# Optimization experiments

Hardware: AMD Instinct MI355X
Metric: run time of the kernel (lower is better)

The kernel has to match this reference:

```python
import jax, jax.numpy as jnp
import numpy as np

B, S, D, H = 2, 2048, 1024, 16
DEPTH = D // H


def setup_inputs() -> dict:
    key = jax.random.key(0)
    ks = jax.random.split(key, 6)
    q = jax.random.normal(ks[0], (B, S, D), dtype=jnp.float32)
    k = jax.random.normal(ks[1], (B, S, D), dtype=jnp.float32)
    v = jax.random.normal(ks[2], (B, S, D), dtype=jnp.float32)
    # causal mask, broadcastable to [B, H, S, S]
    mask = jnp.tril(jnp.ones((S, S), dtype=bool))[None, None, :, :]
    wq = jax.random.normal(ks[3], (D, D), dtype=jnp.float32)
    wk = jax.random.normal(ks[4], (D, D), dtype=jnp.float32)
    wv = jax.random.normal(ks[5], (D, D), dtype=jnp.float32)
    return {"q": q, "k": k, "v": v, "mask": mask, "wq": wq, "wk": wk, "wv": wv}


def _split_heads(x):
    # [B, S, D] -> [B, H, S, depth]
    return x.reshape(x.shape[0], -1, H, DEPTH).transpose(0, 2, 1, 3)


def reference(q, k, v, mask, wq, wk, wv):
    q = _split_heads(q @ wq)
    k = _split_heads(k @ wk)
    v = _split_heads(v @ wv)
    scale = jnp.sqrt(jnp.float32(DEPTH))
    # [B, H, S, S]
    scores = jnp.einsum("bhqd,bhkd->bhqk", q, k) / scale
    scores = jnp.where(mask, scores, jnp.float32(-8.0))
    scores = scores - jnp.max(scores, axis=-1, keepdims=True)
    attn = jax.nn.softmax(scores, axis=-1)
    out = jnp.einsum("bhqk,bhkd->bhqd", attn, v)
    # [B, H, S, depth] -> [B, S, D]
    return out.transpose(0, 2, 1, 3).reshape(out.shape[0], -1, D)
```

## Files before the change

### kernel.cpp

```cpp
#include <hip/hip_runtime.h>
#include <hip/hip_bf16.h>

#define B_  2
#define S_  2048
#define D_  1024
#define H_  16
#define DH_ 64

typedef __attribute__((ext_vector_type(8)))  short  short8;
typedef __attribute__((ext_vector_type(4)))  short  short4b;
typedef __attribute__((ext_vector_type(16))) float  f32x16;

#define MFMA32(A,B,C) __builtin_amdgcn_mfma_f32_32x32x16_bf16(A,B,C,0,0,0)

static __device__ __forceinline__ short bf16b(float x) {
    __hip_bfloat16 h = __float2bfloat16(x);
    return *(short*)&h;
}
static __device__ __forceinline__ float bf16tof(short s) {
    union { unsigned u; float f; } cv;
    cv.u = ((unsigned)(unsigned short)s) << 16;
    return cv.f;
}
static __device__ __forceinline__ void gl2lds(const short* g, short* l) {
    __builtin_amdgcn_global_load_lds(
        (const __attribute__((address_space(1))) unsigned int*)g,
        (__attribute__((address_space(3))) unsigned int*)l, 16, 0, 0);
}

__global__ __launch_bounds__(256)
void conv_x(const float* __restrict__ q, const float* __restrict__ k,
            const float* __restrict__ v, char* __restrict__ ws) {
    const int z = blockIdx.y;
    const float* src = z == 0 ? q : z == 1 ? k : v;
    short* hi = (short*)(ws + (size_t)z * 16777216);
    short* lo = hi + 4194304;
    const int i = (blockIdx.x * 256 + threadIdx.x) * 4;
    float4 xv = *(const float4*)&src[i];
    const float* xf = (const float*)&xv;
    short4b h4, l4;
#pragma unroll
    for (int e = 0; e < 4; ++e) {
        short hb = bf16b(xf[e]);
        h4[e] = hb;
        l4[e] = bf16b(xf[e] - bf16tof(hb));
    }
    *(short4b*)&hi[i] = h4;
    *(short4b*)&lo[i] = l4;
}

__global__ __launch_bounds__(256)
void conv_wT(const float* __restrict__ wq, const float* __restrict__ wk,
             const float* __restrict__ wv, char* __restrict__ ws) {
    __shared__ short HiT[64][80];
    __shared__ short LoT[64][80];
    const int z = blockIdx.z;
    const float* w = z == 0 ? wq : z == 1 ? wk : wv;
    short* oh = (short*)(ws + 50331648 + (size_t)z * 4194304);
    short* ol = oh + 1048576;
    const int t  = threadIdx.x;
    const int k0 = blockIdx.x * 64, n0 = blockIdx.y * 64;

    const int kr = t >> 2, c4 = (t & 3) * 16;
    const float* srow = w + (size_t)(k0 + kr) * 1024 + n0 + c4;
#pragma unroll
    for (int u = 0; u < 16; u += 4) {
        float4 f = *(const float4*)&srow[u];
        const float* ff = (const float*)&f;
#pragma unroll
        for (int e = 0; e < 4; ++e) {
            int nl = c4 + u + e;
            short hb = bf16b(ff[e]);
            HiT[nl][kr] = hb;
            LoT[nl][kr] = bf16b(ff[e] - bf16tof(hb));
        }
    }
    __syncthreads();
    const int nl = t >> 2, kc = (t & 3) * 16;
    size_t off = (size_t)(n0 + nl) * 1024 + k0 + kc;
    *(short8*)&oh[off]     = *(const short8*)&HiT[nl][kc];
    *(short8*)&oh[off + 8] = *(const short8*)&HiT[nl][kc + 8];
    *(short8*)&ol[off]     = *(const short8*)&LoT[nl][kc];
    *(short8*)&ol[off + 8] = *(const short8*)&LoT[nl][kc + 8];
}

#define AHI_ 0
#define ALO_ 4096
#define BHI_ 8192
#define BLO_ 12288

__global__ __launch_bounds__(256, 2)
void proj_mfma(const short* __restrict__ xh0, const short* __restrict__ xl0,
               const short* __restrict__ xh1, const short* __restrict__ xl1,
               const short* __restrict__ xh2, const short* __restrict__ xl2,
               const short* __restrict__ wh0, const short* __restrict__ wl0,
               const short* __restrict__ wh1, const short* __restrict__ wl1,
               const short* __restrict__ wh2, const short* __restrict__ wl2,
               short* __restrict__ qh, short* __restrict__ ql,
               short* __restrict__ kh, short* __restrict__ kl,
               short* __restrict__ vt) {
    __shared__ short lds[16384];
    const int z  = blockIdx.z;
    const int m0 = blockIdx.y * 128;
    const int n0 = blockIdx.x * 128;
    const int t = threadIdx.x, lane = t & 63, w = t >> 6;
    const int l31 = lane & 31, hh = lane >> 5;

    const short* xh = z == 0 ? xh0 : z == 1 ? xh1 : xh2;
    const short* xl = z == 0 ? xl0 : z == 1 ? xl1 : xl2;
    const short* wh = z == 0 ? wh0 : z == 1 ? wh1 : wh2;
    const short* wl = z == 0 ? wl0 : z == 1 ? wl1 : wl2;

    const short* gsrc[8];
    short*       ldst[8];
#pragma unroll
    for (int j = 0; j < 8; ++j) {
        int sub = ((j & 1) << 2) | w;
        int cc  = (sub << 6) | lane;
        int row = cc >> 2, p = cc & 3;
        int kc  = p ^ ((row & 3) ^ ((row >> 2) & 3));
        bool isA  = j < 4;
        bool isHi = (j & 2) == 0;
        const short* base = isA ? (isHi ? xh : xl) : (isHi ? wh : wl);
        int r0g = isA ? m0 : n0;
        gsrc[j] = base + (size_t)(r0g + row) * 1024 + kc * 8;
        ldst[j] = &lds[(j >> 1) * 4096 + sub * 512];
    }

    const int rm0 = ((w & 1) << 6) + l31, rm1 = rm0 + 32;
    const int rn0 = ((w >> 1) << 6) + l31, rn1 = rn0 + 32;
    const int swm = (rm0 & 3) ^ ((rm0 >> 2) & 3);
    const int swn = (rn0 & 3) ^ ((rn0 >> 2) & 3);

    f32x16 accs[2][2] = {};

    for (int kt = 0; kt < 32; ++kt) {
        __syncthreads();
#pragma unroll
        for (int j = 0; j < 8; ++j)
            gl2lds(gsrc[j] + kt * 32, ldst[j]);
        __syncthreads();
#pragma unroll
        for (int ks = 0; ks < 2; ++ks) {
            const int kc = (ks << 1) | hh;
            const int om = (kc ^ swm) << 3;
            const int on = (kc ^ swn) << 3;
            short8 ah0 = *(const short8*)&lds[AHI_ + rm0 * 32 + om];
            short8 ah1 = *(const short8*)&lds[AHI_ + rm1 * 32 + om];
            short8 al0 = *(const short8*)&lds[ALO_ + rm0 * 32 + om];
            short8 al1 = *(const short8*)&lds[ALO_ + rm1 * 32 + om];
            short8 bh0 = *(const short8*)&lds[BHI_ + rn0 * 32 + on];
            short8 bh1 = *(const short8*)&lds[BHI_ + rn1 * 32 + on];
            short8 bl0 = *(const short8*)&lds[BLO_ + rn0 * 32 + on];
            short8 bl1 = *(const short8*)&lds[BLO_ + rn1 * 32 + on];
            accs[0][0] = MFMA32(ah0, bh0, accs[0][0]);
            accs[0][0] = MFMA32(ah0, bl0, accs[0][0]);
            accs[0][0] = MFMA32(al0, bh0, accs[0][0]);
            accs[0][1] = MFMA32(ah0, bh1, accs[0][1]);
            accs[0][1] = MFMA32(ah0, bl1, accs[0][1]);
            accs[0][1] = MFMA32(al0, bh1, accs[0][1]);
            accs[1][0] = MFMA32(ah1, bh0, accs[1][0]);
            accs[1][0] = MFMA32(ah1, bl0, accs[1][0]);
            accs[1][0] = MFMA32(al1, bh0, accs[1][0]);
            accs[1][1] = MFMA32(ah1, bh1, accs[1][1]);
            accs[1][1] = MFMA32(ah1, bl1, accs[1][1]);
            accs[1][1] = MFMA32(al1, bh1, accs[1][1]);
        }
    }

    const int qm = w & 1, qn = w >> 1;
    const int bb = m0 >> 11;
    const int sbase = (m0 & 2047) + qm * 64;
    if (z < 2) {
        short* oh = z == 0 ? qh : kh;
        short* ol = z == 0 ? ql : kl;
#pragma unroll
        for (int mt = 0; mt < 2; ++mt)
#pragma unroll
        for (int nt = 0; nt < 2; ++nt) {
            int n_g = n0 + qn * 64 + nt * 32 + l31;
            int h = n_g >> 6, d = n_g & 63;
#pragma unroll
            for (int r = 0; r < 16; ++r) {
                int s = sbase + mt * 32 + (r & 3) + 8 * (r >> 2) + 4 * hh;
                size_t off = (((size_t)(bb * 16 + h) * 2048 + s) << 6) + d;
                float a = accs[mt][nt][r];
                short hb = bf16b(a);
                oh[off] = hb;
                ol[off] = bf16b(a - bf16tof(hb));
            }
        }
    } else {
#pragma unroll
        for (int mt = 0; mt < 2; ++mt)
#pragma unroll
        for (int nt = 0; nt < 2; ++nt) {
            int n_g = n0 + qn * 64 + nt * 32 + l31;
            int h = n_g >> 6, d = n_g & 63;
            size_t vbase = ((size_t)(bb * 16 + h) * 64 + d) * 2048;
#pragma unroll
            for (int r2 = 0; r2 < 4; ++r2) {
                int s0 = sbase + mt * 32 + 8 * r2 + 4 * hh;
                short4b pk;
#pragma unroll
                for (int a2 = 0; a2 < 4; ++a2)
                    pk[a2] = bf16b(accs[mt][nt][r2 * 4 + a2]);
                *(short4b*)&vt[vbase + s0] = pk;
            }
        }
    }
}

__global__ void vtile_sums(const short* __restrict__ Vt, float* __restrict__ TS) {
    int c = blockIdx.x, bh = blockIdx.y, d = threadIdx.x;
    const short* row = Vt + ((size_t)bh * DH_ + d) * S_ + c * 64;
    float s = 0.f;
    for (int j = 0; j < 64; ++j) s += bf16tof(row[j]);
    TS[((size_t)bh * 32 + c) * 64 + d] = s;
}

__global__ void suffix_scan(const float* __restrict__ TS, float* __restrict__ SV) {
    int bh = blockIdx.x, d = threadIdx.x;
    float run = 0.f;
    for (int c = 32; c >= 0; --c) {
        SV[((size_t)bh * 33 + c) * 64 + d] = run;
        if (c > 0) run += TS[((size_t)bh * 32 + (c - 1)) * 64 + d];
    }
}

__global__ __launch_bounds__(256, 2)
void attn_mfma(const short* __restrict__ Qhi, const short* __restrict__ Qlo,
               const short* __restrict__ Khi, const short* __restrict__ Klo,
               const short* __restrict__ Vt,  const float* __restrict__ SV,
               float* __restrict__ out) {
    __shared__ __align__(16) short KhiS[64 * 72];
    __shared__ __align__(16) short KloS[64 * 72];
    __shared__ __align__(16) short VtS [64 * 72];
    __shared__ __align__(16) short PS  [4][32 * 72];

    const int t     = threadIdx.x;
    const int lane  = t & 63;
    const int w     = t >> 6;
    const int l31   = lane & 31;
    const int hh    = lane >> 5;
    const int bh    = blockIdx.x;
    const int yy    = blockIdx.y;
    const int qt    = (yy < 8) ? yy : 23 - yy;
    const int q0    = qt * 128;
    const int myq   = q0 + w * 32 + l31;
    const int ktend = 2 * qt + 2;

    const size_t basebh = (size_t)bh * S_ * DH_;

    short8 qh[4], ql[4];
    {
        const short* qr = Qhi + basebh + (size_t)myq * DH_;
        const short* lr = Qlo + basebh + (size_t)myq * DH_;
#pragma unroll
        for (int kf = 0; kf < 4; ++kf) {
            int dofs = kf * 16 + hh * 8;
            qh[kf] = *(const short8*)(qr + dofs);
            ql[kf] = *(const short8*)(lr + dofs);
        }
    }

    float m_run = -INFINITY, l_run = 0.f;
    f32x16 oT0 = {}, oT1 = {};

    const int srow = t >> 2;
    const int sc16 = (t & 3) * 16;

    for (int kt = 0; kt < ktend; ++kt) {
        __syncthreads();
        {
            const short* gH = Khi + basebh + (size_t)(kt * 64 + srow) * 64 + sc16;
            const short* gL = Klo + basebh + (size_t)(kt * 64 + srow) * 64 + sc16;
            const short* gV = Vt + (size_t)bh * DH_ * S_ + (size_t)srow * S_ + kt * 64 + sc16;
            short8 a0 = *(const short8*)gH, a1 = *(const short8*)(gH + 8);
            short8 b0 = *(const short8*)gL, b1 = *(const short8*)(gL + 8);
            short8 c0 = *(const short8*)gV, c1 = *(const short8*)(gV + 8);
            *(short8*)&KhiS[srow * 72 + sc16]     = a0;
            *(short8*)&KhiS[srow * 72 + sc16 + 8] = a1;
            *(short8*)&KloS[srow * 72 + sc16]     = b0;
            *(short8*)&KloS[srow * 72 + sc16 + 8] = b1;
            *(short8*)&VtS [srow * 72 + sc16]     = c0;
            *(short8*)&VtS [srow * 72 + sc16 + 8] = c1;
        }
        __syncthreads();

        f32x16 acc0 = {}, acc1 = {};
#pragma unroll
        for (int kf = 0; kf < 4; ++kf) {
            int dofs = kf * 16 + hh * 8;
            short8 k0h = *(const short8*)&KhiS[(l31)      * 72 + dofs];
            short8 k0l = *(const short8*)&KloS[(l31)      * 72 + dofs];
            short8 k1h = *(const short8*)&KhiS[(l31 + 32) * 72 + dofs];
            short8 k1l = *(const short8*)&KloS[(l31 + 32) * 72 + dofs];
            acc0 = MFMA32(k0h, qh[kf], acc0);
            acc0 = MFMA32(k0h, ql[kf], acc0);
            acc0 = MFMA32(k0l, qh[kf], acc0);
            acc1 = MFMA32(k1h, qh[kf], acc1);
            acc1 = MFMA32(k1h, ql[kf], acc1);
            acc1 = MFMA32(k1l, qh[kf], acc1);
        }

        float vals[32];
        float tmax = -INFINITY;
#pragma unroll
        for (int r = 0; r < 16; ++r) {
            int key0 = kt * 64 + ((r & 3) + 8 * (r >> 2) + 4 * hh);
            float v0 = acc0[r] * 0.125f;
            v0 = (key0 <= myq) ? v0 : -8.0f;
            float v1 = acc1[r] * 0.125f;
            v1 = (key0 + 32 <= myq) ? v1 : -8.0f;
            vals[r] = v0;
            vals[16 + r] = v1;
            tmax = fmaxf(tmax, fmaxf(v0, v1));
        }
        tmax = fmaxf(tmax, __shfl_xor(tmax, 32, 64));
        float mnew  = fmaxf(m_run, tmax);
        float alpha = __expf(m_run - mnew);
        float psum  = 0.f;
#pragma unroll
        for (int mt = 0; mt < 2; ++mt)
#pragma unroll
            for (int b2 = 0; b2 < 4; ++b2) {
                short4b pk;
#pragma unroll
                for (int a = 0; a < 4; ++a) {
                    float p = __expf(vals[mt * 16 + b2 * 4 + a] - mnew);
                    short pb = bf16b(p);
                    psum += bf16tof(pb);
                    pk[a] = pb;
                }
                *(short4b*)&PS[w][l31 * 72 + mt * 32 + b2 * 8 + hh * 4] = pk;
            }
        psum += __shfl_xor(psum, 32, 64);
        l_run = l_run * alpha + psum;
        m_run = mnew;
#pragma unroll
        for (int r = 0; r < 16; ++r) { oT0[r] *= alpha; oT1[r] *= alpha; }

#pragma unroll
        for (int kf = 0; kf < 4; ++kf) {
            int kofs = kf * 16 + hh * 8;
            short8 pf = *(const short8*)&PS[w][l31 * 72 + kofs];
            short8 v0 = *(const short8*)&VtS[(l31)      * 72 + kofs];
            short8 v1 = *(const short8*)&VtS[(l31 + 32) * 72 + kofs];
            oT0 = MFMA32(v0, pf, oT0);
            oT1 = MFMA32(v1, pf, oT1);
        }
    }

    {
        float mfin = fmaxf(m_run, -8.0f);
        float aa   = __expf(m_run - mfin);
        float e8   = __expf(-8.0f - mfin);
        float nrem = (float)(S_ - ktend * 64);
        float lfin = l_run * aa + nrem * e8;
        float inv  = 1.0f / lfin;
        const float* sv = SV + ((size_t)bh * 33 + ktend) * 64;
#pragma unroll
        for (int r = 0; r < 16; ++r) {
            int dim0 = (r & 3) + 8 * (r >> 2) + 4 * hh;
            oT0[r] = (oT0[r] * aa + e8 * sv[dim0])      * inv;
            oT1[r] = (oT1[r] * aa + e8 * sv[dim0 + 32]) * inv;
        }
    }

    __syncthreads();
    float* Ob = (w == 0) ? (float*)KhiS :
                (w == 1) ? (float*)KloS :
                (w == 2) ? (float*)VtS  : (float*)PS;
#pragma unroll
    for (int r = 0; r < 16; ++r) {
        int dim0 = (r & 3) + 8 * (r >> 2) + 4 * hh;
        Ob[l31 * 68 + dim0]      = oT0[r];
        Ob[l31 * 68 + dim0 + 32] = oT1[r];
    }
    {
        const int qq = lane >> 1;
        const int ch = (lane & 1) * 32;
        const float* src = Ob + qq * 68 + ch;
        const int b  = bh >> 4;
        const int h  = bh & 15;
        float* dst = out + ((size_t)b * S_ + (q0 + w * 32 + qq)) * D_ + h * 64 + ch;
#pragma unroll
        for (int c = 0; c < 32; c += 4)
            *(float4*)(dst + c) = *(const float4*)(src + c);
    }
}

extern "C" void kernel_launch(void* const* d_in, const int* in_sizes, int n_in,
                              void* d_out, int out_size, void* d_ws, size_t ws_size,
                              hipStream_t stream) {
    const float* q  = (const float*)d_in[0];
    const float* k  = (const float*)d_in[1];
    const float* v  = (const float*)d_in[2];
    const float* wq = (const float*)d_in[4];
    const float* wk = (const float*)d_in[5];
    const float* wv = (const float*)d_in[6];
    float* out = (float*)d_out;

    char* ws = (char*)d_ws;
    const short* XH[3] = {(short*)ws, (short*)(ws + 16777216), (short*)(ws + 33554432)};
    const short* XL[3] = {XH[0] + 4194304, XH[1] + 4194304, XH[2] + 4194304};
    const short* WH[3] = {(short*)(ws + 50331648), (short*)(ws + 54525952), (short*)(ws + 58720256)};
    const short* WL[3] = {WH[0] + 1048576, WH[1] + 1048576, WH[2] + 1048576};
    float* TS = (float*)(ws + 62914560);
    float* SV = (float*)(ws + 62914560 + 262144);

    short* Qhi = (short*)d_in[0]; short* Qlo = Qhi + 4194304;
    short* Khi = (short*)d_in[1]; short* Klo = Khi + 4194304;
    short* Vt  = (short*)d_in[2];

    conv_x <<<dim3(4096, 3), 256, 0, stream>>>(q, k, v, ws);
    conv_wT<<<dim3(16, 16, 3), 256, 0, stream>>>(wq, wk, wv, ws);

    proj_mfma<<<dim3(8, 32, 3), 256, 0, stream>>>(
        XH[0], XL[0], XH[1], XL[1], XH[2], XL[2],
        WH[0], WL[0], WH[1], WL[1], WH[2], WL[2],
        Qhi, Qlo, Khi, Klo, Vt);

    vtile_sums<<<dim3(32, 32), 64, 0, stream>>>(Vt, TS);
    suffix_scan<<<32, 64, 0, stream>>>(TS, SV);

    attn_mfma<<<dim3(32, 16), 256, 0, stream>>>(Qhi, Qlo, Khi, Klo, Vt, SV, out);
}
```

Measured before the change: 285.6 us.

## Stage projection epilogue through LDS, remap grid, and double query rows per attention wave

The projection kernel now uses a 1D grid with a grouped tile order for L2 reuse. Its epilogue stages outputs through shared memory so global stores become coalesced 16-byte writes instead of scattered 2-byte ones. The attention kernel is rewritten so each wave handles 64 query rows with 128 threads per block and XOR-swizzled unpadded LDS. This halves K/V tile loads per query and lets the largest causal tiles launch first. vtile_sums is vectorized. The costs are higher register pressure, fewer waves per block and extra syncs in the epilogue.

```diff
diff --git a/kernel.cpp b/kernel.cpp
--- a/kernel.cpp
+++ b/kernel.cpp
@@ -99,10 +99,12 @@
                short* __restrict__ qh, short* __restrict__ ql,
                short* __restrict__ kh, short* __restrict__ kl,
                short* __restrict__ vt) {
-    __shared__ short lds[16384];
-    const int z  = blockIdx.z;
-    const int m0 = blockIdx.y * 128;
-    const int n0 = blockIdx.x * 128;
+    __shared__ short lds[17408];
+    const int id = blockIdx.x;
+    const int z  = id >> 8;
+    const int rr = id & 255;
+    const int m0 = ((((rr >> 6) << 3) | (rr & 7))) * 128;
+    const int n0 = ((rr >> 3) & 7) * 128;
     const int t = threadIdx.x, lane = t & 63, w = t >> 6;
     const int l31 = lane & 31, hh = lane >> 5;
 
@@ -168,45 +170,62 @@
         }
     }
 
-    const int qm = w & 1, qn = w >> 1;
+    __syncthreads();
     const int bb = m0 >> 11;
-    const int sbase = (m0 & 2047) + qm * 64;
+    const int sm = m0 & 2047;
+    const int srw = t >> 1, hf = t & 1;
+
     if (z < 2) {
         short* oh = z == 0 ? qh : kh;
         short* ol = z == 0 ? ql : kl;
 #pragma unroll
+        for (int pass = 0; pass < 2; ++pass) {
+#pragma unroll
+            for (int mt = 0; mt < 2; ++mt)
+#pragma unroll
+            for (int nt = 0; nt < 2; ++nt) {
+                int ncol = ((w >> 1) << 6) + (nt << 5) + l31;
+#pragma unroll
+                for (int r = 0; r < 16; ++r) {
+                    int srl = ((w & 1) << 6) + (mt << 5) + (r & 3) + 8 * (r >> 2) + 4 * hh;
+                    float a = accs[mt][nt][r];
+                    short hb = bf16b(a);
+                    lds[srl * 136 + ncol] = (pass == 0) ? hb : bf16b(a - bf16tof(hb));
+                }
+            }
+            __syncthreads();
+            {
+                short* op = (pass == 0) ? oh : ol;
+                const short* src = &lds[srw * 136 + (hf << 6)];
+                int hI = (n0 >> 6) + hf;
+                size_t off = (((size_t)(bb * 16 + hI) * 2048) + sm + srw) << 6;
+#pragma unroll
+                for (int j = 0; j < 8; ++j)
+                    *(short8*)&op[off + (j << 3)] = *(const short8*)(src + (j << 3));
+            }
+            __syncthreads();
+        }
+    } else {
+#pragma unroll
         for (int mt = 0; mt < 2; ++mt)
 #pragma unroll
         for (int nt = 0; nt < 2; ++nt) {
-            int n_g = n0 + qn * 64 + nt * 32 + l31;
-            int h = n_g >> 6, d = n_g & 63;
+            int ncol = ((w >> 1) << 6) + (nt << 5) + l31;
 #pragma unroll
             for (int r = 0; r < 16; ++r) {
-                int s = sbase + mt * 32 + (r & 3) + 8 * (r >> 2) + 4 * hh;
-                size_t off = (((size_t)(bb * 16 + h) * 2048 + s) << 6) + d;
-                float a = accs[mt][nt][r];
-                short hb = bf16b(a);
-                oh[off] = hb;
-                ol[off] = bf16b(a - bf16tof(hb));
-            }
-        }
-    } else {
-#pragma unroll
-        for (int mt = 0; mt < 2; ++mt)
-#pragma unroll
-        for (int nt = 0; nt < 2; ++nt) {
-            int n_g = n0 + qn * 64 + nt * 32 + l31;
-            int h = n_g >> 6, d = n_g & 63;
-            size_t vbase = ((size_t)(bb * 16 + h) * 64 + d) * 2048;
-#pragma unroll
-            for (int r2 = 0; r2 < 4; ++r2) {
-                int s0 = sbase + mt * 32 + 8 * r2 + 4 * hh;
-                short4b pk;
-#pragma unroll
-                for (int a2 = 0; a2 < 4; ++a2)
-                    pk[a2] = bf16b(accs[mt][nt][r2 * 4 + a2]);
-                *(short4b*)&vt[vbase + s0] = pk;
-            }
+                int srl = ((w & 1) << 6) + (mt << 5) + (r & 3) + 8 * (r >> 2) + 4 * hh;
+                lds[ncol * 136 + srl] = bf16b(accs[mt][nt][r]);
+            }
+        }
+        __syncthreads();
+        {
+            int hI = (n0 + srw) >> 6;
+            int d  = (n0 + srw) & 63;
+            const short* src = &lds[srw * 136 + (hf << 6)];
+            size_t off = (((size_t)(bb * 16 + hI) * 64) + d) * 2048 + sm + (hf << 6);
+#pragma unroll
+            for (int j = 0; j < 8; ++j)
+                *(short8*)&vt[off + (j << 3)] = *(const short8*)(src + (j << 3));
         }
     }
 }
@@ -215,7 +234,12 @@
     int c = blockIdx.x, bh = blockIdx.y, d = threadIdx.x;
     const short* row = Vt + ((size_t)bh * DH_ + d) * S_ + c * 64;
     float s = 0.f;
-    for (int j = 0; j < 64; ++j) s += bf16tof(row[j]);
+#pragma unroll
+    for (int j8 = 0; j8 < 8; ++j8) {
+        short8 v8 = *(const short8*)(row + j8 * 8);
+#pragma unroll
+        for (int e = 0; e < 8; ++e) s += bf16tof(v8[e]);
+    }
     TS[((size_t)bh * 32 + c) * 64 + d] = s;
 }
 
@@ -228,163 +252,174 @@
     }
 }
 
-__global__ __launch_bounds__(256, 2)
-void attn_mfma(const short* __restrict__ Qhi, const short* __restrict__ Qlo,
-               const short* __restrict__ Khi, const short* __restrict__ Klo,
-               const short* __restrict__ Vt,  const float* __restrict__ SV,
-               float* __restrict__ out) {
-    __shared__ __align__(16) short KhiS[64 * 72];
-    __shared__ __align__(16) short KloS[64 * 72];
-    __shared__ __align__(16) short VtS [64 * 72];
-    __shared__ __align__(16) short PS  [4][32 * 72];
-
-    const int t     = threadIdx.x;
-    const int lane  = t & 63;
-    const int w     = t >> 6;
-    const int l31   = lane & 31;
-    const int hh    = lane >> 5;
-    const int bh    = blockIdx.x;
-    const int yy    = blockIdx.y;
-    const int qt    = (yy < 8) ? yy : 23 - yy;
-    const int q0    = qt * 128;
-    const int myq   = q0 + w * 32 + l31;
+__global__ __launch_bounds__(128, 2)
+void attn_mfma2(const short* __restrict__ Qhi, const short* __restrict__ Qlo,
+                const short* __restrict__ Khi, const short* __restrict__ Klo,
+                const short* __restrict__ Vt,  const float* __restrict__ SV,
+                float* __restrict__ out) {
+    __shared__ __align__(16) short smem[20480];
+    short* KhiS = smem;
+    short* KloS = smem + 4096;
+    short* VtS  = smem + 8192;
+    short* PS   = smem + 12288;
+
+    const int t = threadIdx.x, lane = t & 63, w = t >> 6;
+    const int l31 = lane & 31, hh = lane >> 5;
+    const int bh = blockIdx.x;
+    const int qt = 15 - blockIdx.y;
+    const int q0 = qt * 128;
     const int ktend = 2 * qt + 2;
-
-    const size_t basebh = (size_t)bh * S_ * DH_;
-
-    short8 qh[4], ql[4];
-    {
-        const short* qr = Qhi + basebh + (size_t)myq * DH_;
-        const short* lr = Qlo + basebh + (size_t)myq * DH_;
+    const size_t basebh = (size_t)bh * (S_ * DH_);
+
+    short8 qfh[2][4], qfl[2][4];
+#pragma unroll
+    for (int qb = 0; qb < 2; ++qb) {
+        const short* qr = Qhi + basebh + ((size_t)(q0 + (w << 6) + (qb << 5) + l31) << 6);
+        const short* lr = Qlo + basebh + ((size_t)(q0 + (w << 6) + (qb << 5) + l31) << 6);
 #pragma unroll
         for (int kf = 0; kf < 4; ++kf) {
             int dofs = kf * 16 + hh * 8;
-            qh[kf] = *(const short8*)(qr + dofs);
-            ql[kf] = *(const short8*)(lr + dofs);
-        }
-    }
-
-    float m_run = -INFINITY, l_run = 0.f;
-    f32x16 oT0 = {}, oT1 = {};
-
-    const int srow = t >> 2;
-    const int sc16 = (t & 3) * 16;
+            qfh[qb][kf] = *(const short8*)(qr + dofs);
+            qfl[qb][kf] = *(const short8*)(lr + dofs);
+        }
+    }
+
+    float m_run[2] = {-INFINITY, -INFINITY}, l_run[2] = {0.f, 0.f};
+    f32x16 accO[2][2] = {};
+
+    const int srow = t >> 1;
+    const int cb   = (t & 1) * 2;
+    const int sw   = srow & 3;
 
     for (int kt = 0; kt < ktend; ++kt) {
         __syncthreads();
         {
-            const short* gH = Khi + basebh + (size_t)(kt * 64 + srow) * 64 + sc16;
-            const short* gL = Klo + basebh + (size_t)(kt * 64 + srow) * 64 + sc16;
-            const short* gV = Vt + (size_t)bh * DH_ * S_ + (size_t)srow * S_ + kt * 64 + sc16;
-            short8 a0 = *(const short8*)gH, a1 = *(const short8*)(gH + 8);
-            short8 b0 = *(const short8*)gL, b1 = *(const short8*)(gL + 8);
-            short8 c0 = *(const short8*)gV, c1 = *(const short8*)(gV + 8);
-            *(short8*)&KhiS[srow * 72 + sc16]     = a0;
-            *(short8*)&KhiS[srow * 72 + sc16 + 8] = a1;
-            *(short8*)&KloS[srow * 72 + sc16]     = b0;
-            *(short8*)&KloS[srow * 72 + sc16 + 8] = b1;
-            *(short8*)&VtS [srow * 72 + sc16]     = c0;
-            *(short8*)&VtS [srow * 72 + sc16 + 8] = c1;
+            const short* gH = Khi + basebh + ((size_t)(kt * 64 + srow) << 6) + cb * 16;
+            const short* gL = Klo + basebh + ((size_t)(kt * 64 + srow) << 6) + cb * 16;
+            const short* gV = Vt + basebh + ((size_t)srow << 11) + kt * 64 + cb * 16;
+#pragma unroll
+            for (int c2 = 0; c2 < 2; ++c2) {
+                int pos = (((cb + c2) ^ sw) << 4);
+                *(short8*)&KhiS[(srow << 6) + pos]     = *(const short8*)(gH + c2 * 16);
+                *(short8*)&KhiS[(srow << 6) + pos + 8] = *(const short8*)(gH + c2 * 16 + 8);
+                *(short8*)&KloS[(srow << 6) + pos]     = *(const short8*)(gL + c2 * 16);
+                *(short8*)&KloS[(srow << 6) + pos + 8] = *(const short8*)(gL + c2 * 16 + 8);
+                *(short8*)&VtS [(srow << 6) + pos]     = *(const short8*)(gV + c2 * 16);
+                *(short8*)&VtS [(srow << 6) + pos + 8] = *(const short8*)(gV + c2 * 16 + 8);
+            }
         }
         __syncthreads();
 
-        f32x16 acc0 = {}, acc1 = {};
+        f32x16 accS[2][2] = {};
 #pragma unroll
         for (int kf = 0; kf < 4; ++kf) {
-            int dofs = kf * 16 + hh * 8;
-            short8 k0h = *(const short8*)&KhiS[(l31)      * 72 + dofs];
-            short8 k0l = *(const short8*)&KloS[(l31)      * 72 + dofs];
-            short8 k1h = *(const short8*)&KhiS[(l31 + 32) * 72 + dofs];
-            short8 k1l = *(const short8*)&KloS[(l31 + 32) * 72 + dofs];
-            acc0 = MFMA32(k0h, qh[kf], acc0);
-            acc0 = MFMA32(k0h, ql[kf], acc0);
-            acc0 = MFMA32(k0l, qh[kf], acc0);
-            acc1 = MFMA32(k1h, qh[kf], acc1);
-            acc1 = MFMA32(k1h, ql[kf], acc1);
-            acc1 = MFMA32(k1l, qh[kf], acc1);
-        }
-
-        float vals[32];
-        float tmax = -INFINITY;
-#pragma unroll
-        for (int r = 0; r < 16; ++r) {
-            int key0 = kt * 64 + ((r & 3) + 8 * (r >> 2) + 4 * hh);
-            float v0 = acc0[r] * 0.125f;
-            v0 = (key0 <= myq) ? v0 : -8.0f;
-            float v1 = acc1[r] * 0.125f;
-            v1 = (key0 + 32 <= myq) ? v1 : -8.0f;
-            vals[r] = v0;
-            vals[16 + r] = v1;
-            tmax = fmaxf(tmax, fmaxf(v0, v1));
-        }
-        tmax = fmaxf(tmax, __shfl_xor(tmax, 32, 64));
-        float mnew  = fmaxf(m_run, tmax);
-        float alpha = __expf(m_run - mnew);
-        float psum  = 0.f;
-#pragma unroll
-        for (int mt = 0; mt < 2; ++mt)
+            const int po = ((kf ^ (l31 & 3)) << 4) + (hh << 3);
+            short8 k0h = *(const short8*)&KhiS[(l31 << 6)        + po];
+            short8 k1h = *(const short8*)&KhiS[((l31 + 32) << 6) + po];
+            short8 k0l = *(const short8*)&KloS[(l31 << 6)        + po];
+            short8 k1l = *(const short8*)&KloS[((l31 + 32) << 6) + po];
+#pragma unroll
+            for (int qb = 0; qb < 2; ++qb) {
+                accS[qb][0] = MFMA32(k0h, qfh[qb][kf], accS[qb][0]);
+                accS[qb][0] = MFMA32(k0h, qfl[qb][kf], accS[qb][0]);
+                accS[qb][0] = MFMA32(k0l, qfh[qb][kf], accS[qb][0]);
+                accS[qb][1] = MFMA32(k1h, qfh[qb][kf], accS[qb][1]);
+                accS[qb][1] = MFMA32(k1h, qfl[qb][kf], accS[qb][1]);
+                accS[qb][1] = MFMA32(k1l, qfh[qb][kf], accS[qb][1]);
+            }
+        }
+
+#pragma unroll
+        for (int qb = 0; qb < 2; ++qb) {
+            const int myq = q0 + (w << 6) + (qb << 5) + l31;
+            float vals[32];
+            float tmax = -INFINITY;
+#pragma unroll
+            for (int r = 0; r < 16; ++r) {
+                int key0 = kt * 64 + ((r & 3) + 8 * (r >> 2) + 4 * hh);
+                float v0 = accS[qb][0][r] * 0.125f;
+                v0 = (key0 <= myq) ? v0 : -8.0f;
+                float v1 = accS[qb][1][r] * 0.125f;
+                v1 = (key0 + 32 <= myq) ? v1 : -8.0f;
+                vals[r] = v0;
+                vals[16 + r] = v1;
+                tmax = fmaxf(tmax, fmaxf(v0, v1));
+            }
+            tmax = fmaxf(tmax, __shfl_xor(tmax, 32, 64));
+            float mnew  = fmaxf(m_run[qb], tmax);
+            float alpha = __expf(m_run[qb] - mnew);
+            float psum  = 0.f;
+            short* psrow = &PS[(w << 12) + (((qb << 5) + l31) << 6)];
+#pragma unroll
+            for (int kb = 0; kb < 2; ++kb)
 #pragma unroll
             for (int b2 = 0; b2 < 4; ++b2) {
                 short4b pk;
 #pragma unroll
                 for (int a = 0; a < 4; ++a) {
-                    float p = __expf(vals[mt * 16 + b2 * 4 + a] - mnew);
+                    float p = __expf(vals[kb * 16 + b2 * 4 + a] - mnew);
                     short pb = bf16b(p);
                     psum += bf16tof(pb);
                     pk[a] = pb;
                 }
-                *(short4b*)&PS[w][l31 * 72 + mt * 32 + b2 * 8 + hh * 4] = pk;
-            }
-        psum += __shfl_xor(psum, 32, 64);
-        l_run = l_run * alpha + psum;
-        m_run = mnew;
-#pragma unroll
-        for (int r = 0; r < 16; ++r) { oT0[r] *= alpha; oT1[r] *= alpha; }
+                int chunk = (((kb << 1) | (b2 >> 1)) ^ (l31 & 3));
+                *(short4b*)&psrow[(chunk << 4) + ((b2 & 1) << 3) + (hh << 2)] = pk;
+            }
+            psum += __shfl_xor(psum, 32, 64);
+            l_run[qb] = l_run[qb] * alpha + psum;
+            m_run[qb] = mnew;
+#pragma unroll
+            for (int r = 0; r < 16; ++r) { accO[qb][0][r] *= alpha; accO[qb][1][r] *= alpha; }
+        }
 
 #pragma unroll
         for (int kf = 0; kf < 4; ++kf) {
-            int kofs = kf * 16 + hh * 8;
-            short8 pf = *(const short8*)&PS[w][l31 * 72 + kofs];
-            short8 v0 = *(const short8*)&VtS[(l31)      * 72 + kofs];
-            short8 v1 = *(const short8*)&VtS[(l31 + 32) * 72 + kofs];
-            oT0 = MFMA32(v0, pf, oT0);
-            oT1 = MFMA32(v1, pf, oT1);
-        }
-    }
-
-    {
-        float mfin = fmaxf(m_run, -8.0f);
-        float aa   = __expf(m_run - mfin);
+            const int po = ((kf ^ (l31 & 3)) << 4) + (hh << 3);
+            short8 v0 = *(const short8*)&VtS[(l31 << 6)        + po];
+            short8 v1 = *(const short8*)&VtS[((l31 + 32) << 6) + po];
+#pragma unroll
+            for (int qb = 0; qb < 2; ++qb) {
+                short8 pf = *(const short8*)&PS[(w << 12) + (((qb << 5) + l31) << 6) + po];
+                accO[qb][0] = MFMA32(v0, pf, accO[qb][0]);
+                accO[qb][1] = MFMA32(v1, pf, accO[qb][1]);
+            }
+        }
+    }
+
+#pragma unroll
+    for (int qb = 0; qb < 2; ++qb) {
+        float mfin = fmaxf(m_run[qb], -8.0f);
+        float aa   = __expf(m_run[qb] - mfin);
         float e8   = __expf(-8.0f - mfin);
         float nrem = (float)(S_ - ktend * 64);
-        float lfin = l_run * aa + nrem * e8;
+        float lfin = l_run[qb] * aa + nrem * e8;
         float inv  = 1.0f / lfin;
         const float* sv = SV + ((size_t)bh * 33 + ktend) * 64;
 #pragma unroll
         for (int r = 0; r < 16; ++r) {
             int dim0 = (r & 3) + 8 * (r >> 2) + 4 * hh;
-            oT0[r] = (oT0[r] * aa + e8 * sv[dim0])      * inv;
-            oT1[r] = (oT1[r] * aa + e8 * sv[dim0 + 32]) * inv;
+            accO[qb][0][r] = (accO[qb][0][r] * aa + e8 * sv[dim0])      * inv;
+            accO[qb][1][r] = (accO[qb][1][r] * aa + e8 * sv[dim0 + 32]) * inv;
         }
     }
 
     __syncthreads();
-    float* Ob = (w == 0) ? (float*)KhiS :
-                (w == 1) ? (float*)KloS :
-                (w == 2) ? (float*)VtS  : (float*)PS;
+    float* Ob = (float*)smem + w * 4352;
+#pragma unroll
+    for (int qb = 0; qb < 2; ++qb)
 #pragma unroll
     for (int r = 0; r < 16; ++r) {
         int dim0 = (r & 3) + 8 * (r >> 2) + 4 * hh;
-        Ob[l31 * 68 + dim0]      = oT0[r];
-        Ob[l31 * 68 + dim0 + 32] = oT1[r];
-    }
-    {
-        const int qq = lane >> 1;
-        const int ch = (lane & 1) * 32;
-        const float* src = Ob + qq * 68 + ch;
-        const int b  = bh >> 4;
-        const int h  = bh & 15;
-        float* dst = out + ((size_t)b * S_ + (q0 + w * 32 + qq)) * D_ + h * 64 + ch;
+        Ob[((qb << 5) + l31) * 68 + dim0]      = accO[qb][0][r];
+        Ob[((qb << 5) + l31) * 68 + dim0 + 32] = accO[qb][1][r];
+    }
+    const int b = bh >> 4, h = bh & 15;
+#pragma unroll
+    for (int it = 0; it < 2; ++it) {
+        int qrow = (it << 5) + (lane >> 1);
+        int chh  = (lane & 1) << 5;
+        const float* src = Ob + qrow * 68 + chh;
+        float* dst = out + ((size_t)b * S_ + q0 + (w << 6) + qrow) * D_ + (h << 6) + chh;
 #pragma unroll
         for (int c = 0; c < 32; c += 4)
             *(float4*)(dst + c) = *(const float4*)(src + c);
@@ -417,7 +452,7 @@
     conv_x <<<dim3(4096, 3), 256, 0, stream>>>(q, k, v, ws);
     conv_wT<<<dim3(16, 16, 3), 256, 0, stream>>>(wq, wk, wv, ws);
 
-    proj_mfma<<<dim3(8, 32, 3), 256, 0, stream>>>(
+    proj_mfma<<<768, 256, 0, stream>>>(
         XH[0], XL[0], XH[1], XL[1], XH[2], XL[2],
         WH[0], WL[0], WH[1], WL[1], WH[2], WL[2],
         Qhi, Qlo, Khi, Klo, Vt);
@@ -425,5 +460,5 @@
     vtile_sums<<<dim3(32, 32), 64, 0, stream>>>(Vt, TS);
     suffix_scan<<<32, 64, 0, stream>>>(TS, SV);
 
-    attn_mfma<<<dim3(32, 16), 256, 0, stream>>>(Qhi, Qlo, Khi, Klo, Vt, SV, out);
-}
+    attn_mfma2<<<dim3(32, 16), 128, 0, stream>>>(Qhi, Qlo, Khi, Klo, Vt, SV, out);
+}
```

After: 326.6 us. 14.3% more time.
